# Kernel tuning notes

Measured on AMD Instinct MI355X. Metric: run time of the kernel, lower is better.

Reference implementation:

```python
import jax, jax.numpy as jnp
import numpy as np

B, S, D = 32, 2048, 1024
E, K = 64, 8
N_TAGS = 128


def setup_inputs() -> dict:
    key = jax.random.key(0)
    k1, k2, k3, k4, k5, k6 = jax.random.split(key, 6)
    hidden_states = jax.random.normal(k1, (B, S, D), dtype=jnp.float32)
    subw_indices = jax.random.randint(k2, (B, E, K), 0, S, dtype=jnp.int32)
    subw_counts = jax.random.randint(k3, (B, E), 1, K + 1, dtype=jnp.int32)
    num_entities = jax.random.randint(k4, (B,), 1, E + 1, dtype=jnp.int32)
    fc_w = jax.random.normal(k5, (N_TAGS, D), dtype=jnp.float32) * (1.0 / np.sqrt(D))
    fc_b = jax.random.normal(k6, (N_TAGS,), dtype=jnp.float32) * 0.01
    return {
        "hidden_states": hidden_states,
        "subw_indices": subw_indices,
        "subw_counts": subw_counts,
        "num_entities": num_entities,
        "fc_w": fc_w,
        "fc_b": fc_b,
    }


def reference(hidden_states, subw_indices, subw_counts, num_entities, fc_w, fc_b):
    # Gather subword embeddings: [B, E, K, D]
    flat_idx = subw_indices.reshape(B, E * K)                      # [B, E*K]
    gathered = jnp.take_along_axis(
        hidden_states, flat_idx[:, :, None], axis=1
    ).reshape(B, E, K, D)
    # Mask padded subword slots and mean-pool per entity
    subw_mask = (jnp.arange(K)[None, None, :] < subw_counts[:, :, None])  # [B,E,K]
    subw_mask = subw_mask.astype(hidden_states.dtype)
    ent_emb = jnp.einsum("bekd,bek->bed", gathered, subw_mask)
    ent_emb = ent_emb / subw_counts[:, :, None].astype(hidden_states.dtype)
    # Zero-pad entities past num_entities (original pads with zero_emb)
    ent_mask = (jnp.arange(E)[None, :] < num_entities[:, None])    # [B,E]
    ent_emb = ent_emb * ent_mask[:, :, None].astype(hidden_states.dtype)
    # fc applied to all positions (padded rows yield the bias, as in original)
    logits = jnp.einsum("bed,td->bet", ent_emb, fc_w) + fc_b
    return logits
```

## Files before the change

### kernel.cpp

```cpp
#include <hip/hip_runtime.h>

#define BB 32
#define SS 2048
#define DD 1024
#define EE 64
#define KK 8
#define TT 128

__global__ __launch_bounds__(256) void pool_kernel(
    const float* __restrict__ hs,
    const int*   __restrict__ subw_idx,
    const int*   __restrict__ subw_cnt,
    const int*   __restrict__ num_ent,
    const float* __restrict__ fc_b,
    float*       __restrict__ ent,
    float*       __restrict__ out)
{
    const int be = blockIdx.x;
    const int b  = be >> 6;
    const int e  = be & 63;
    const int t  = threadIdx.x;

    const int cnt = subw_cnt[be];
    const int ne  = num_ent[b];
    const float scale = (e < ne) ? (1.0f / (float)cnt) : 0.0f;

    const int* idxp = subw_idx + (size_t)be * KK;

    float4 acc = make_float4(0.f, 0.f, 0.f, 0.f);
    #pragma unroll
    for (int k = 0; k < KK; ++k) {
        if (k < cnt) {
            const int s = idxp[k];
            const float4* row = (const float4*)(hs + ((size_t)b * SS + s) * DD);
            float4 v = row[t];
            acc.x += v.x; acc.y += v.y; acc.z += v.z; acc.w += v.w;
        }
    }
    acc.x *= scale; acc.y *= scale; acc.z *= scale; acc.w *= scale;
    ((float4*)(ent + (size_t)be * DD))[t] = acc;

    const int gid = be * 256 + t;
    if (gid < BB * EE * TT) {
        out[gid] = fc_b[gid & (TT - 1)];
    }
}

#define M_TILE 16
#define KSPLIT 4
#define KCH   (DD / KSPLIT)
#define KSUB  32

__global__ __launch_bounds__(256) void fc_kernel(
    const float* __restrict__ ent,
    const float* __restrict__ fc_w,
    float*       __restrict__ out)
{
    __shared__ float Al[M_TILE][KSUB];
    __shared__ float Wl[TT][KSUB + 1];

    const int bx    = blockIdx.x;
    const int mtile = bx >> 2;
    const int ks    = bx & (KSPLIT - 1);
    const int t     = threadIdx.x;
    const int n     = t & (TT - 1);
    const int m0    = (t >> 7) * 8;

    const int k0 = ks * KCH;

    float acc[8] = {0.f, 0.f, 0.f, 0.f, 0.f, 0.f, 0.f, 0.f};

    for (int kc = 0; kc < KCH; kc += KSUB) {
        const int kbase = k0 + kc;

        #pragma unroll
        for (int i = t; i < M_TILE * KSUB; i += 256) {
            const int mm = i >> 5, kk = i & 31;
            Al[mm][kk] = ent[(size_t)(mtile * M_TILE + mm) * DD + kbase + kk];
        }
        #pragma unroll
        for (int i = t * 4; i < TT * KSUB; i += 256 * 4) {
            const int tag = i >> 5, kk = i & 31;
            float4 w = *(const float4*)(fc_w + (size_t)tag * DD + kbase + kk);
            Wl[tag][kk + 0] = w.x;
            Wl[tag][kk + 1] = w.y;
            Wl[tag][kk + 2] = w.z;
            Wl[tag][kk + 3] = w.w;
        }
        __syncthreads();

        #pragma unroll
        for (int kk = 0; kk < KSUB; ++kk) {
            const float w = Wl[n][kk];
            #pragma unroll
            for (int m = 0; m < 8; ++m)
                acc[m] += Al[m0 + m][kk] * w;
        }
        __syncthreads();
    }

    #pragma unroll
    for (int m = 0; m < 8; ++m)
        atomicAdd(&out[(size_t)(mtile * M_TILE + m0 + m) * TT + n], acc[m]);
}

extern "C" void kernel_launch(void* const* d_in, const int* in_sizes, int n_in,
                              void* d_out, int out_size, void* d_ws, size_t ws_size,
                              hipStream_t stream) {
    const float* hs       = (const float*)d_in[0];
    const int*   subw_idx = (const int*)  d_in[1];
    const int*   subw_cnt = (const int*)  d_in[2];
    const int*   num_ent  = (const int*)  d_in[3];
    const float* fc_w     = (const float*)d_in[4];
    const float* fc_b     = (const float*)d_in[5];
    float*       out      = (float*)d_out;
    float*       ent      = (float*)d_ws;

    pool_kernel<<<BB * EE, 256, 0, stream>>>(hs, subw_idx, subw_cnt, num_ent,
                                             fc_b, ent, out);
    fc_kernel<<<(BB * EE / M_TILE) * KSPLIT, 256, 0, stream>>>(ent, fc_w, out);
}
```

Measured before the change: 350.6 us.

## Compute entity FC with bf16 MFMA and split-K partials instead of FP32 atomics

The pooling kernel now writes entity embeddings and a copy of fc_w as bf16. The FC GEMM uses 16x16x32 bf16 MFMA instructions with an 8-way K split, writing partial sums to workspace. A separate reduce kernel sums the partials and adds the bias, replacing the atomicAdd epilogue. This trades FP32 accuracy for bf16 inputs and adds a third launch plus partial-buffer traffic. The gather in the pooling stage, which is probably the dominant cost, is left unchanged.

```diff
diff --git a/kernel.cpp b/kernel.cpp
--- a/kernel.cpp
+++ b/kernel.cpp
@@ -6,15 +6,29 @@
 #define EE 64
 #define KK 8
 #define TT 128
+#define MM (BB * EE)
+
+#define KSPLIT 8
+#define KCHUNK (DD / KSPLIT)
+#define MT 32
+
+typedef __attribute__((ext_vector_type(8))) short short8;
+typedef __attribute__((ext_vector_type(4))) float f32x4;
+
+__device__ __forceinline__ unsigned short f2bf(float f) {
+    union { float f; unsigned int u; } v; v.f = f;
+    unsigned int u = v.u + 0x7FFFu + ((v.u >> 16) & 1u);
+    return (unsigned short)(u >> 16);
+}
 
 __global__ __launch_bounds__(256) void pool_kernel(
     const float* __restrict__ hs,
     const int*   __restrict__ subw_idx,
     const int*   __restrict__ subw_cnt,
     const int*   __restrict__ num_ent,
-    const float* __restrict__ fc_b,
-    float*       __restrict__ ent,
-    float*       __restrict__ out)
+    const float* __restrict__ fc_w,
+    unsigned short* __restrict__ entb,
+    unsigned short* __restrict__ wb)
 {
     const int be = blockIdx.x;
     const int b  = be >> 6;
@@ -37,71 +51,97 @@
             acc.x += v.x; acc.y += v.y; acc.z += v.z; acc.w += v.w;
         }
     }
-    acc.x *= scale; acc.y *= scale; acc.z *= scale; acc.w *= scale;
-    ((float4*)(ent + (size_t)be * DD))[t] = acc;
+    ushort4 o;
+    o.x = f2bf(acc.x * scale); o.y = f2bf(acc.y * scale);
+    o.z = f2bf(acc.z * scale); o.w = f2bf(acc.w * scale);
+    *(ushort4*)(entb + (size_t)be * DD + 4 * t) = o;
 
-    const int gid = be * 256 + t;
-    if (gid < BB * EE * TT) {
-        out[gid] = fc_b[gid & (TT - 1)];
+    if (t < 64) {
+        const int j = be * 64 + t;
+        wb[j] = f2bf(fc_w[j]);
     }
 }
 
-#define M_TILE 16
-#define KSPLIT 4
-#define KCH   (DD / KSPLIT)
-#define KSUB  32
+__global__ __launch_bounds__(256) void fc_mfma_kernel(
+    const unsigned short* __restrict__ entb,
+    const unsigned short* __restrict__ wb,
+    float* __restrict__ part)
+{
+    __shared__ unsigned short As[MT][32];
+    __shared__ unsigned short Bs[TT][32];
 
-__global__ __launch_bounds__(256) void fc_kernel(
-    const float* __restrict__ ent,
-    const float* __restrict__ fc_w,
-    float*       __restrict__ out)
-{
-    __shared__ float Al[M_TILE][KSUB];
-    __shared__ float Wl[TT][KSUB + 1];
+    const int bx = blockIdx.x;
+    const int mt = bx >> 3;
+    const int ks = bx & (KSPLIT - 1);
+    const int t  = threadIdx.x;
+    const int wid  = t >> 6;
+    const int lane = t & 63;
 
-    const int bx    = blockIdx.x;
-    const int mtile = bx >> 2;
-    const int ks    = bx & (KSPLIT - 1);
-    const int t     = threadIdx.x;
-    const int n     = t & (TT - 1);
-    const int m0    = (t >> 7) * 8;
+    const int msub  = (wid & 1) * 16;
+    const int nbase = (wid >> 1) * 64;
 
-    const int k0 = ks * KCH;
+    const int k0 = ks * KCHUNK;
 
-    float acc[8] = {0.f, 0.f, 0.f, 0.f, 0.f, 0.f, 0.f, 0.f};
+    f32x4 acc0 = {0.f,0.f,0.f,0.f}, acc1 = {0.f,0.f,0.f,0.f};
+    f32x4 acc2 = {0.f,0.f,0.f,0.f}, acc3 = {0.f,0.f,0.f,0.f};
 
-    for (int kc = 0; kc < KCH; kc += KSUB) {
-        const int kbase = k0 + kc;
+    const int lm = lane & 15;
+    const int lq = (lane >> 4) * 8;
 
-        #pragma unroll
-        for (int i = t; i < M_TILE * KSUB; i += 256) {
-            const int mm = i >> 5, kk = i & 31;
-            Al[mm][kk] = ent[(size_t)(mtile * M_TILE + mm) * DD + kbase + kk];
+    for (int kc = 0; kc < KCHUNK; kc += 32) {
+        if (t < 128) {
+            const int m = t >> 2, s = t & 3;
+            *(float4*)&As[m][s * 8] =
+                *(const float4*)(entb + (size_t)(mt * MT + m) * DD + k0 + kc + s * 8);
         }
         #pragma unroll
-        for (int i = t * 4; i < TT * KSUB; i += 256 * 4) {
-            const int tag = i >> 5, kk = i & 31;
-            float4 w = *(const float4*)(fc_w + (size_t)tag * DD + kbase + kk);
-            Wl[tag][kk + 0] = w.x;
-            Wl[tag][kk + 1] = w.y;
-            Wl[tag][kk + 2] = w.z;
-            Wl[tag][kk + 3] = w.w;
+        for (int j = 0; j < 2; ++j) {
+            const int i = t + j * 256;
+            const int n = i >> 2, s = i & 3;
+            *(float4*)&Bs[n][s * 8] =
+                *(const float4*)(wb + (size_t)n * DD + k0 + kc + s * 8);
         }
         __syncthreads();
 
-        #pragma unroll
-        for (int kk = 0; kk < KSUB; ++kk) {
-            const float w = Wl[n][kk];
-            #pragma unroll
-            for (int m = 0; m < 8; ++m)
-                acc[m] += Al[m0 + m][kk] * w;
-        }
+        short8 a = *(const short8*)&As[msub + lm][lq];
+        short8 b0 = *(const short8*)&Bs[nbase +  0 + lm][lq];
+        short8 b1 = *(const short8*)&Bs[nbase + 16 + lm][lq];
+        short8 b2 = *(const short8*)&Bs[nbase + 32 + lm][lq];
+        short8 b3 = *(const short8*)&Bs[nbase + 48 + lm][lq];
+
+        acc0 = __builtin_amdgcn_mfma_f32_16x16x32_bf16(a, b0, acc0, 0, 0, 0);
+        acc1 = __builtin_amdgcn_mfma_f32_16x16x32_bf16(a, b1, acc1, 0, 0, 0);
+        acc2 = __builtin_amdgcn_mfma_f32_16x16x32_bf16(a, b2, acc2, 0, 0, 0);
+        acc3 = __builtin_amdgcn_mfma_f32_16x16x32_bf16(a, b3, acc3, 0, 0, 0);
         __syncthreads();
     }
 
+    float* outp = part + (size_t)ks * MM * TT;
+    const int mrow = mt * MT + msub + (lane >> 4) * 4;
+    const int ncol = nbase + (lane & 15);
     #pragma unroll
-    for (int m = 0; m < 8; ++m)
-        atomicAdd(&out[(size_t)(mtile * M_TILE + m0 + m) * TT + n], acc[m]);
+    for (int r = 0; r < 4; ++r) {
+        const size_t base = (size_t)(mrow + r) * TT + ncol;
+        outp[base +  0] = acc0[r];
+        outp[base + 16] = acc1[r];
+        outp[base + 32] = acc2[r];
+        outp[base + 48] = acc3[r];
+    }
+}
+
+__global__ __launch_bounds__(256) void reduce_kernel(
+    const float* __restrict__ part,
+    const float* __restrict__ fc_b,
+    float* __restrict__ out)
+{
+    const int i = blockIdx.x * 256 + threadIdx.x;
+    float4 s = *(const float4*)(fc_b + (i & 31) * 4);
+    #pragma unroll
+    for (int k = 0; k < KSPLIT; ++k) {
+        float4 p = *(const float4*)(part + (size_t)k * MM * TT + 4 * i);
+        s.x += p.x; s.y += p.y; s.z += p.z; s.w += p.w;
+    }
+    *(float4*)(out + 4 * (size_t)i) = s;
 }
 
 extern "C" void kernel_launch(void* const* d_in, const int* in_sizes, int n_in,
@@ -114,9 +154,13 @@
     const float* fc_w     = (const float*)d_in[4];
     const float* fc_b     = (const float*)d_in[5];
     float*       out      = (float*)d_out;
-    float*       ent      = (float*)d_ws;
 
-    pool_kernel<<<BB * EE, 256, 0, stream>>>(hs, subw_idx, subw_cnt, num_ent,
-                                             fc_b, ent, out);
-    fc_kernel<<<(BB * EE / M_TILE) * KSPLIT, 256, 0, stream>>>(ent, fc_w, out);
+    unsigned short* entb = (unsigned short*)d_ws;
+    unsigned short* wb   = (unsigned short*)((char*)d_ws + (size_t)MM * DD * 2);
+    float*          part = (float*)((char*)d_ws + (size_t)MM * DD * 2 + (size_t)TT * DD * 2);
+
+    pool_kernel<<<MM, 256, 0, stream>>>(hs, subw_idx, subw_cnt, num_ent,
+                                        fc_w, entb, wb);
+    fc_mfma_kernel<<<(MM / MT) * KSPLIT, 256, 0, stream>>>(entb, wb, part);
+    reduce_kernel<<<(MM * TT / 4) / 256, 256, 0, stream>>>(part, fc_b, out);
 }
```

Result: faster. 318.4 us (-9.2%).

## Fuse pooling and FC into one kernel using bf16 MFMA

Applied to the files above, without the earlier changes.

Merges the gather/mean-pool kernel and the FC GEMM into one kernel. Each block pools 8 entities into shared memory as bf16, then computes their logits with 16x16x32 bf16 MFMA against fc_w, which is converted to bf16 chunk by chunk. This removes the intermediate ent buffer round trip, the second launch, the split-K atomics and the separate bias pre-initialisation. In exchange, fc_w is re-read and re-converted by each of the 256 blocks, and bf16 rounding lowers precision.

```diff
diff --git a/kernel.cpp b/kernel.cpp
--- a/kernel.cpp
+++ b/kernel.cpp
@@ -6,102 +6,121 @@
 #define EE 64
 #define KK 8
 #define TT 128
+#define MM (BB * EE)
 
-__global__ __launch_bounds__(256) void pool_kernel(
+#define MT 8
+#define KC 128
+#define ASTR 1032
+#define WSTR 136
+
+typedef __attribute__((ext_vector_type(8))) short short8;
+typedef __attribute__((ext_vector_type(4))) float f32x4;
+
+__device__ __forceinline__ unsigned short f2bf(float f) {
+    union { float f; unsigned int u; } v; v.f = f;
+    unsigned int u = v.u + 0x7FFFu + ((v.u >> 16) & 1u);
+    return (unsigned short)(u >> 16);
+}
+
+__global__ __launch_bounds__(256) void te_fused_kernel(
     const float* __restrict__ hs,
     const int*   __restrict__ subw_idx,
     const int*   __restrict__ subw_cnt,
     const int*   __restrict__ num_ent,
+    const float* __restrict__ fc_w,
     const float* __restrict__ fc_b,
-    float*       __restrict__ ent,
-    float*       __restrict__ out)
+    float* __restrict__ out)
 {
-    const int be = blockIdx.x;
-    const int b  = be >> 6;
-    const int e  = be & 63;
-    const int t  = threadIdx.x;
+    __shared__ unsigned short As[MT][ASTR];
+    __shared__ unsigned short Ws[TT][WSTR];
 
-    const int cnt = subw_cnt[be];
-    const int ne  = num_ent[b];
-    const float scale = (e < ne) ? (1.0f / (float)cnt) : 0.0f;
+    const int mt   = blockIdx.x;
+    const int t    = threadIdx.x;
+    const int wid  = t >> 6;
+    const int lane = t & 63;
 
-    const int* idxp = subw_idx + (size_t)be * KK;
+    {
+        const int r  = t >> 5;
+        const int c  = t & 31;
+        const int be = mt * MT + r;
+        const int b  = be >> 6;
+        const int e  = be & 63;
+        const int cnt = subw_cnt[be];
+        const int ne  = num_ent[b];
+        const float scale = (e < ne) ? (1.0f / (float)cnt) : 0.0f;
+        const int* idxp = subw_idx + (size_t)be * KK;
 
-    float4 acc = make_float4(0.f, 0.f, 0.f, 0.f);
-    #pragma unroll
-    for (int k = 0; k < KK; ++k) {
-        if (k < cnt) {
+        float4 acc4[8];
+        #pragma unroll
+        for (int j = 0; j < 8; ++j) acc4[j] = make_float4(0.f, 0.f, 0.f, 0.f);
+
+        for (int k = 0; k < cnt; ++k) {
             const int s = idxp[k];
             const float4* row = (const float4*)(hs + ((size_t)b * SS + s) * DD);
-            float4 v = row[t];
-            acc.x += v.x; acc.y += v.y; acc.z += v.z; acc.w += v.w;
+            #pragma unroll
+            for (int j = 0; j < 8; ++j) {
+                float4 v = row[j * 32 + c];
+                acc4[j].x += v.x; acc4[j].y += v.y;
+                acc4[j].z += v.z; acc4[j].w += v.w;
+            }
+        }
+        #pragma unroll
+        for (int j = 0; j < 8; ++j) {
+            ushort4 o;
+            o.x = f2bf(acc4[j].x * scale); o.y = f2bf(acc4[j].y * scale);
+            o.z = f2bf(acc4[j].z * scale); o.w = f2bf(acc4[j].w * scale);
+            *(ushort4*)&As[r][(j * 32 + c) * 4] = o;
         }
     }
-    acc.x *= scale; acc.y *= scale; acc.z *= scale; acc.w *= scale;
-    ((float4*)(ent + (size_t)be * DD))[t] = acc;
 
-    const int gid = be * 256 + t;
-    if (gid < BB * EE * TT) {
-        out[gid] = fc_b[gid & (TT - 1)];
-    }
-}
+    const int nbase = wid * 32;
+    const int lm  = lane & 15;
+    const int lq  = (lane >> 4) * 8;
+    const int lmA = lm & 7;
 
-#define M_TILE 16
-#define KSPLIT 4
-#define KCH   (DD / KSPLIT)
-#define KSUB  32
+    f32x4 acc0 = {0.f,0.f,0.f,0.f}, acc1 = {0.f,0.f,0.f,0.f};
 
-__global__ __launch_bounds__(256) void fc_kernel(
-    const float* __restrict__ ent,
-    const float* __restrict__ fc_w,
-    float*       __restrict__ out)
-{
-    __shared__ float Al[M_TILE][KSUB];
-    __shared__ float Wl[TT][KSUB + 1];
+    const int n = t >> 1;
+    const int h = (t & 1) * 64;
 
-    const int bx    = blockIdx.x;
-    const int mtile = bx >> 2;
-    const int ks    = bx & (KSPLIT - 1);
-    const int t     = threadIdx.x;
-    const int n     = t & (TT - 1);
-    const int m0    = (t >> 7) * 8;
-
-    const int k0 = ks * KCH;
-
-    float acc[8] = {0.f, 0.f, 0.f, 0.f, 0.f, 0.f, 0.f, 0.f};
-
-    for (int kc = 0; kc < KCH; kc += KSUB) {
-        const int kbase = k0 + kc;
-
-        #pragma unroll
-        for (int i = t; i < M_TILE * KSUB; i += 256) {
-            const int mm = i >> 5, kk = i & 31;
-            Al[mm][kk] = ent[(size_t)(mtile * M_TILE + mm) * DD + kbase + kk];
-        }
-        #pragma unroll
-        for (int i = t * 4; i < TT * KSUB; i += 256 * 4) {
-            const int tag = i >> 5, kk = i & 31;
-            float4 w = *(const float4*)(fc_w + (size_t)tag * DD + kbase + kk);
-            Wl[tag][kk + 0] = w.x;
-            Wl[tag][kk + 1] = w.y;
-            Wl[tag][kk + 2] = w.z;
-            Wl[tag][kk + 3] = w.w;
+    for (int kc = 0; kc < DD / KC; ++kc) {
+        __syncthreads();
+        {
+            const float4* wrow = (const float4*)(fc_w + (size_t)n * DD + kc * KC + h);
+            #pragma unroll
+            for (int j = 0; j < 16; ++j) {
+                float4 v = wrow[j];
+                ushort4 o;
+                o.x = f2bf(v.x); o.y = f2bf(v.y);
+                o.z = f2bf(v.z); o.w = f2bf(v.w);
+                *(ushort4*)&Ws[n][h + j * 4] = o;
+            }
         }
         __syncthreads();
 
         #pragma unroll
-        for (int kk = 0; kk < KSUB; ++kk) {
-            const float w = Wl[n][kk];
-            #pragma unroll
-            for (int m = 0; m < 8; ++m)
-                acc[m] += Al[m0 + m][kk] * w;
+        for (int kstep = 0; kstep < KC / 32; ++kstep) {
+            const int ko = kstep * 32 + lq;
+            short8 a  = *(const short8*)&As[lmA][kc * KC + ko];
+            short8 b0 = *(const short8*)&Ws[nbase +  0 + lm][ko];
+            short8 b1 = *(const short8*)&Ws[nbase + 16 + lm][ko];
+            acc0 = __builtin_amdgcn_mfma_f32_16x16x32_bf16(a, b0, acc0, 0, 0, 0);
+            acc1 = __builtin_amdgcn_mfma_f32_16x16x32_bf16(a, b1, acc1, 0, 0, 0);
         }
-        __syncthreads();
     }
 
-    #pragma unroll
-    for (int m = 0; m < 8; ++m)
-        atomicAdd(&out[(size_t)(mtile * M_TILE + m0 + m) * TT + n], acc[m]);
+    if (lane < 32) {
+        const int mrow = mt * MT + (lane >> 4) * 4;
+        const int c0 = nbase + lm;
+        const float b0v = fc_b[c0];
+        const float b1v = fc_b[c0 + 16];
+        #pragma unroll
+        for (int r = 0; r < 4; ++r) {
+            float* o = out + (size_t)(mrow + r) * TT + c0;
+            o[0]  = acc0[r] + b0v;
+            o[16] = acc1[r] + b1v;
+        }
+    }
 }
 
 extern "C" void kernel_launch(void* const* d_in, const int* in_sizes, int n_in,
@@ -114,9 +133,7 @@
     const float* fc_w     = (const float*)d_in[4];
     const float* fc_b     = (const float*)d_in[5];
     float*       out      = (float*)d_out;
-    float*       ent      = (float*)d_ws;
 
-    pool_kernel<<<BB * EE, 256, 0, stream>>>(hs, subw_idx, subw_cnt, num_ent,
-                                             fc_b, ent, out);
-    fc_kernel<<<(BB * EE / M_TILE) * KSPLIT, 256, 0, stream>>>(ent, fc_w, out);
+    te_fused_kernel<<<MM / MT, 256, 0, stream>>>(
+        hs, subw_idx, subw_cnt, num_ent, fc_w, fc_b, out);
 }
```

Result: faster. 327.5 us (-6.6%).
